# Kernel optimization log

Measured on AMD Instinct MI355X. Metric: run time of the kernel, lower is better.

Reference implementation:

```python
import jax, jax.numpy as jnp
import numpy as np

ROPE_THETA = 500000.0


def apply_rope(x, position_ids):
    # x: (B, H, S, hd), position_ids: (B, S)
    hd = x.shape[-1]
    inv_freq = 1.0 / (ROPE_THETA ** (jnp.arange(0, hd, 2, dtype=x.dtype) / hd))  # (hd/2,)
    freqs = position_ids.astype(x.dtype)[:, :, None] * inv_freq  # (B, S, hd/2)
    sin = jnp.sin(freqs)[:, None, :, :]  # (B, 1, S, hd/2)
    cos = jnp.cos(freqs)[:, None, :, :]
    x1 = x[..., ::2]
    x2 = x[..., 1::2]
    even = x1 * cos - x2 * sin
    odd = x2 * cos + x1 * sin
    # interleave even/odd back: stack on a new trailing axis then flatten
    return jnp.stack([even, odd], axis=-1).reshape(x.shape)


def setup_inputs() -> dict:
    key = jax.random.key(0)
    k_x, k_q, k_k, k_v, k_o = jax.random.split(key, 5)
    B, S, D = 2, 2048, 2048
    H, H_kv = 32, 8
    hd = D // H
    x = jax.random.normal(k_x, (B, S, D), dtype=jnp.float32)
    position_ids = jnp.broadcast_to(jnp.arange(S, dtype=jnp.int64)[None, :], (B, S))
    scale = 0.02
    Wq = jax.random.normal(k_q, (D, H * hd), dtype=jnp.float32) * scale
    Wk = jax.random.normal(k_k, (D, H_kv * hd), dtype=jnp.float32) * scale
    Wv = jax.random.normal(k_v, (D, H_kv * hd), dtype=jnp.float32) * scale
    Wo = jax.random.normal(k_o, (D, D), dtype=jnp.float32) * scale
    return {"x": x, "position_ids": position_ids, "Wq": Wq, "Wk": Wk, "Wv": Wv, "Wo": Wo}


def reference(x, position_ids, Wq, Wk, Wv, Wo):
    B, S, D = x.shape
    H, H_kv = 32, 8
    hd = D // H
    G = H // H_kv  # query heads per kv head

    q = (x @ Wq).reshape(B, S, H, hd).transpose(0, 2, 1, 3)        # (B, H, S, hd)
    k = (x @ Wk).reshape(B, S, H_kv, hd).transpose(0, 2, 1, 3)     # (B, H_kv, S, hd)
    v = (x @ Wv).reshape(B, S, H_kv, hd).transpose(0, 2, 1, 3)

    q = apply_rope(q, position_ids)
    k = apply_rope(k, position_ids)

    # GQA: group query heads (B, H_kv, G, S, hd); repeat_interleave maps head h -> kv head h // G
    qg = q.reshape(B, H_kv, G, S, hd)
    scores = jnp.einsum("bkgsh,bkth->bkgst", qg, k) / jnp.sqrt(jnp.asarray(hd, x.dtype))

    causal = jnp.triu(jnp.ones((S, S), dtype=bool), 1)  # True = masked
    scores = jnp.where(causal, jnp.asarray(-jnp.inf, scores.dtype), scores)

    attn = jax.nn.softmax(scores, axis=-1)  # (B, H_kv, G, S, S)
    z = jnp.einsum("bkgst,bkth->bkgsh", attn, v)  # (B, H_kv, G, S, hd)
    z = z.reshape(B, H, S, hd).transpose(0, 2, 1, 3).reshape(B, S, D)
    return z @ Wo
```

## Files before the change

### kernel.cpp

```cpp
#include <hip/hip_runtime.h>
#include <hip/hip_bf16.h>


#define S_LEN 2048
#define DIM   2048
#define NH    32
#define NKV   8
#define HD    64
#define BS    4096
#define NQKV  3072
#define LL(x) ((long long)(x))

typedef __bf16 bf16x8 __attribute__((ext_vector_type(8)));
typedef float  f32x4  __attribute__((ext_vector_type(4)));
typedef float  f32x16 __attribute__((ext_vector_type(16)));
typedef unsigned u32x4 __attribute__((ext_vector_type(4)));

__device__ __forceinline__ unsigned short bfb(float f) {
  __hip_bfloat16 h = __float2bfloat16(f);
  return *reinterpret_cast<unsigned short*>(&h);
}

__device__ __forceinline__ unsigned cvtpk(float lo, float hi) {
  unsigned u;
  asm("v_cvt_pk_bf16_f32 %0, %1, %2" : "=v"(u) : "v"(lo), "v"(hi));
  return u;
}

__device__ __forceinline__ void gload16(const void* g, void* l) {
  __builtin_amdgcn_global_load_lds(
      (const __attribute__((address_space(1))) void*)g,
      (__attribute__((address_space(3))) void*)l, 16, 0, 0);
}

__device__ __forceinline__ void tcast_body(
    const float* __restrict__ in, unsigned short* __restrict__ out,
    int K, int N, int bx, int by, int tid, float* tile ) {
  int n0 = bx * 32, k0 = by * 32;
  int tx = tid & 31, ty = tid >> 5;
#pragma unroll
  for (int r = 0; r < 32; r += 8)
    tile[(ty + r) * 33 + tx] = in[LL(k0 + ty + r) * N + n0 + tx];
  __syncthreads();
#pragma unroll
  for (int r = 0; r < 32; r += 8)
    out[LL(n0 + ty + r) * K + k0 + tx] = bfb(tile[tx * 33 + ty + r]);
}

__global__ __launch_bounds__(256) void k_prep(
    const float* __restrict__ x,  const float* __restrict__ Wq,
    const float* __restrict__ Wk, const float* __restrict__ Wv,
    const float* __restrict__ Wo, float* __restrict__ tab,
    unsigned short* __restrict__ xb, unsigned short* __restrict__ wqkvt,
    unsigned short* __restrict__ wot) {
  __shared__ float tile[32 * 33];
  int blk = blockIdx.x, tid = threadIdx.x;
  if (blk < 256) {
    int i = blk * 256 + tid;
    int s = i >> 5, f = i & 31;
    double inv = pow(500000.0, -2.0 * (double)f / 64.0);
    double fr = (double)s * inv;
    tab[2 * i]     = (float)cos(fr);
    tab[2 * i + 1] = (float)sin(fr);
  } else if (blk < 8448) {
    int i = (blk - 256) * 256 + tid;
    float4 v = ((const float4*)x)[i];
    ushort4 o;
    o.x = bfb(v.x); o.y = bfb(v.y); o.z = bfb(v.z); o.w = bfb(v.w);
    ((ushort4*)xb)[i] = o;
  } else if (blk < 12544) {
    int t2 = blk - 8448;
    tcast_body(Wq, wqkvt, DIM, DIM, t2 & 63, t2 >> 6, tid, tile);
  } else if (blk < 13568) {
    int t3 = blk - 12544;
    tcast_body(Wk, wqkvt + LL(2048) * DIM, DIM, 512, t3 & 15, t3 >> 4, tid, tile);
  } else if (blk < 14592) {
    int t4 = blk - 13568;
    tcast_body(Wv, wqkvt + LL(2560) * DIM, DIM, 512, t4 & 15, t4 >> 4, tid, tile);
  } else {
    int t5 = blk - 14592;
    tcast_body(Wo, wot, DIM, DIM, t5 & 63, t5 >> 6, tid, tile);
  }
}

template <int MODE>
__global__ __launch_bounds__(256, 2) void k_gemm(
    const unsigned short* __restrict__ A, const unsigned short* __restrict__ Bt,
    void* __restrict__ Cout, int M, int N, int K,
    const float* __restrict__ tab, unsigned short* __restrict__ qbuf,
    unsigned short* __restrict__ kbuf, unsigned short* __restrict__ vtb) {
  __shared__ __align__(16) unsigned short As[128 * 32];
  __shared__ __align__(16) unsigned short Bs[128 * 32];
  int t = threadIdx.x;
  int lane = t & 63, w = t >> 6;
  int wr = w >> 1, wc = w & 1;
  int g = lane >> 4, r = lane & 15;
  int gx = gridDim.x;
  int nwg = gx * gridDim.y;
  int lin = blockIdx.y * gx + blockIdx.x;
  int cpx = nwg >> 3;
  int swz = (lin & 7) * cpx + (lin >> 3);
  int bx = swz % gx, by = swz / gx;
  long long rowBase = LL(by) * 128;
  long long colBase = LL(bx) * 128;

  f32x4 acc[4][4] = {};

  int c0 = t, c1 = t + 256;
  const unsigned short* ag0 = A + (rowBase + (c0 >> 2)) * K + (c0 & 3) * 8;
  const unsigned short* ag1 = A + (rowBase + (c1 >> 2)) * K + (c1 & 3) * 8;
  const unsigned short* bg0 = Bt + (colBase + (c0 >> 2)) * K + (c0 & 3) * 8;
  const unsigned short* bg1 = Bt + (colBase + (c1 >> 2)) * K + (c1 & 3) * 8;
  char* lA0 = (char*)As + c0 * 16; char* lA1 = (char*)As + c1 * 16;
  char* lB0 = (char*)Bs + c0 * 16; char* lB1 = (char*)Bs + c1 * 16;

  for (int kt = 0; kt < K; kt += 32) {
    __syncthreads();
    gload16(ag0 + kt, lA0);
    gload16(ag1 + kt, lA1);
    gload16(bg0 + kt, lB0);
    gload16(bg1 + kt, lB1);
    __syncthreads();

    bf16x8 af[4], bfr[4];
#pragma unroll
    for (int m = 0; m < 4; m++)
      af[m] = *(const bf16x8*)(const void*)(As + (wr * 64 + m * 16 + r) * 32 + g * 8);
#pragma unroll
    for (int n = 0; n < 4; n++)
      bfr[n] = *(const bf16x8*)(const void*)(Bs + (wc * 64 + n * 16 + r) * 32 + g * 8);
#pragma unroll
    for (int m = 0; m < 4; m++)
#pragma unroll
      for (int n = 0; n < 4; n++)
        acc[m][n] = __builtin_amdgcn_mfma_f32_16x16x32_bf16(af[m], bfr[n], acc[m][n], 0, 0, 0);
  }

  if (MODE == 0) {
#pragma unroll
    for (int m = 0; m < 4; m++)
#pragma unroll
      for (int n = 0; n < 4; n++) {
        long long row0 = rowBase + wr * 64 + m * 16 + g * 4;
        long long col = colBase + wc * 64 + n * 16 + r;
#pragma unroll
        for (int j = 0; j < 4; j++)
          ((float*)Cout)[(row0 + j) * N + col] = acc[m][n][j];
      }
  } else {
#pragma unroll
    for (int n = 0; n < 4; n++) {
      int gc0 = (int)colBase + wc * 64 + n * 16;
      int gc = gc0 + r;
      if (gc0 < 2560) {
        unsigned short* dst; int dcol, dstride; float scale;
        if (gc0 < 2048) { dst = qbuf; dcol = gc;        dstride = DIM; scale = 0.18033688f; }
        else            { dst = kbuf; dcol = gc - 2048; dstride = 512; scale = 1.0f; }
        int f = (gc & 63) >> 1;
        float sgn = (gc & 1) ? 1.f : -1.f;
#pragma unroll
        for (int m = 0; m < 4; m++) {
          long long row0 = rowBase + wr * 64 + m * 16 + g * 4;
#pragma unroll
          for (int j = 0; j < 4; j++) {
            float v = acc[m][n][j];
            float part = __shfl_xor(v, 1);
            int s = (int)((row0 + j) & (S_LEN - 1));
            float cc = tab[(s * 32 + f) * 2], ss = tab[(s * 32 + f) * 2 + 1];
            float o = (v * cc + sgn * part * ss) * scale;
            dst[(row0 + j) * dstride + dcol] = bfb(o);
          }
        }
      } else {
        int dcol = gc - 2560;
#pragma unroll
        for (int m = 0; m < 4; m++) {
          long long row0 = rowBase + wr * 64 + m * 16 + g * 4;
#pragma unroll
          for (int j = 0; j < 4; j++) {
            long long row = row0 + j;
            long long bq = row >> 11;
            int s = (int)(row & (S_LEN - 1));
            vtb[(bq * 512 + dcol) * S_LEN + s] = bfb(acc[m][n][j]);
          }
        }
      }
    }
  }
}

__global__ __launch_bounds__(256, 2) void k_attn(
    const unsigned short* __restrict__ qb, const unsigned short* __restrict__ kb,
    const unsigned short* __restrict__ vt, unsigned short* __restrict__ zb) {
  int lin = blockIdx.x + 16 * (blockIdx.y + 32 * blockIdx.z);
  int kvh = lin & 7;
  int idx = lin >> 3;
  int st = 15 - (idx >> 3);
  int b = (idx >> 2) & 1;
  int h = kvh * 4 + (idx & 3);
  int bh = b * NKV + kvh;

  int t = threadIdx.x, lane = t & 63, w = t >> 6;
  int l31 = lane & 31, hi = lane >> 5;
  int sw = (l31 & 7) * 8;

  __shared__ __align__(16) unsigned short Ks[2][64 * 64];
  __shared__ __align__(16) unsigned short Vs[2][64 * 64];

  int c0 = t, c1 = t + 256;
  const unsigned short* kg0 = kb + LL(b) * S_LEN * 512 + (c0 >> 3) * 512 + kvh * HD
                                 + (((c0 & 7) ^ ((c0 >> 3) & 7)) * 8);
  const unsigned short* kg1 = kb + LL(b) * S_LEN * 512 + (c1 >> 3) * 512 + kvh * HD
                                 + (((c1 & 7) ^ ((c1 >> 3) & 7)) * 8);
  const unsigned short* vg0 = vt + (LL(bh) * HD + (c0 >> 3)) * S_LEN
                                 + (((c0 & 7) ^ ((c0 >> 3) & 7)) * 8);
  const unsigned short* vg1 = vt + (LL(bh) * HD + (c1 >> 3)) * S_LEN
                                 + (((c1 & 7) ^ ((c1 >> 3) & 7)) * 8);

#define STAGE(bufi, kst_)                                              \
  {                                                                    \
    gload16(kg0 + LL(kst_) * 512, (char*)Ks[bufi] + c0 * 16);          \
    gload16(kg1 + LL(kst_) * 512, (char*)Ks[bufi] + c1 * 16);          \
    gload16(vg0 + (kst_), (char*)Vs[bufi] + c0 * 16);                  \
    gload16(vg1 + (kst_), (char*)Vs[bufi] + c1 * 16);                  \
  }

  int rowb = st * 128 + w * 32;
  int qg = rowb + l31;
  long long qrow = LL(b) * S_LEN + qg;

  bf16x8 qf[4];
#pragma unroll
  for (int s = 0; s < 4; s++)
    qf[s] = *(const bf16x8*)(const void*)(qb + qrow * DIM + h * HD + s * 16 + hi * 8);

  f32x16 acc0 = {}, acc1 = {};
  float mrun = -1e30f, lrun = 0.f;

  int nt = 2 * st + 2;
  STAGE(0, 0);
  for (int tt = 0; tt < nt; tt++) {
    int kst = tt * 64;
    int cur = tt & 1;
    asm volatile("s_waitcnt vmcnt(0)" ::: "memory");
    __builtin_amdgcn_s_barrier();
    __builtin_amdgcn_sched_barrier(0);
    if (tt + 1 < nt) STAGE(cur ^ 1, kst + 64);

    if (kst <= rowb + 31) {
      const unsigned short* Kc = Ks[cur];
      const unsigned short* Vc = Vs[cur];

      bf16x8 kf[2][4];
#pragma unroll
      for (int kbi = 0; kbi < 2; kbi++)
#pragma unroll
        for (int s = 0; s < 4; s++)
          kf[kbi][s] = *(const bf16x8*)(const void*)(
              Kc + (kbi * 32 + l31) * 64 + ((s * 16 + hi * 8) ^ sw));

      __builtin_amdgcn_s_setprio(1);
      f32x16 sc0 = {}, sc1 = {};
#pragma unroll
      for (int s = 0; s < 4; s++) {
        sc0 = __builtin_amdgcn_mfma_f32_32x32x16_bf16(kf[0][s], qf[s], sc0, 0, 0, 0);
        sc1 = __builtin_amdgcn_mfma_f32_32x32x16_bf16(kf[1][s], qf[s], sc1, 0, 0, 0);
      }
      __builtin_amdgcn_s_setprio(0);

      bf16x8 vf[8];
#pragma unroll
      for (int db = 0; db < 2; db++)
#pragma unroll
        for (int f = 0; f < 4; f++)
          vf[db * 4 + f] = *(const bf16x8*)(const void*)(
              Vc + (db * 32 + l31) * 64 + ((f * 16 + hi * 8) ^ sw));

      if (kst + 63 > rowb) {
#pragma unroll
        for (int q = 0; q < 16; q++) {
          int kl = (q & 3) + 8 * (q >> 2) + 4 * hi;
          if (kst + kl > qg) sc0[q] = -1e30f;
          if (kst + 32 + kl > qg) sc1[q] = -1e30f;
        }
      }

      float pm = -1e30f;
#pragma unroll
      for (int q = 0; q < 16; q++) {
        pm = fmaxf(pm, sc0[q]);
        pm = fmaxf(pm, sc1[q]);
      }
      pm = fmaxf(pm, __shfl_xor(pm, 32));
      if (__any(pm > mrun + 12.0f)) {
        float mnew = fmaxf(mrun, pm);
        float al = exp2f(mrun - mnew);
        mrun = mnew;
        lrun *= al;
        acc0 *= al;
        acc1 *= al;
      }
      f32x16 pv0, pv1;
      float ls = 0.f;
#pragma unroll
      for (int q = 0; q < 16; q++) {
        pv0[q] = exp2f(sc0[q] - mrun);
        pv1[q] = exp2f(sc1[q] - mrun);
        ls += pv0[q] + pv1[q];
      }
      lrun += ls + __shfl_xor(ls, 32);

      bf16x8 pfr[4];
#pragma unroll
      for (int f = 0; f < 4; f++) {
        int qb_ = (f & 1) * 8;
        float e0, e1, e2, e3, e4, e5, e6, e7;
        if (f < 2) {
          e0 = pv0[qb_ + 0]; e1 = pv0[qb_ + 1]; e2 = pv0[qb_ + 2]; e3 = pv0[qb_ + 3];
          e4 = pv0[qb_ + 4]; e5 = pv0[qb_ + 5]; e6 = pv0[qb_ + 6]; e7 = pv0[qb_ + 7];
        } else {
          e0 = pv1[qb_ + 0]; e1 = pv1[qb_ + 1]; e2 = pv1[qb_ + 2]; e3 = pv1[qb_ + 3];
          e4 = pv1[qb_ + 4]; e5 = pv1[qb_ + 5]; e6 = pv1[qb_ + 6]; e7 = pv1[qb_ + 7];
        }
        unsigned a0 = cvtpk(e0, e1), a1 = cvtpk(e2, e3);
        unsigned b0 = cvtpk(e4, e5), b1 = cvtpk(e6, e7);
        asm volatile("v_permlane32_swap_b32 %0, %1" : "+v"(a0), "+v"(b0));
        asm volatile("v_permlane32_swap_b32 %0, %1" : "+v"(a1), "+v"(b1));
        u32x4 uu;
        uu[0] = a0;
        uu[1] = a1;
        uu[2] = b0;
        uu[3] = b1;
        pfr[f] = *(bf16x8*)&uu;
      }

      __builtin_amdgcn_s_setprio(1);
#pragma unroll
      for (int f = 0; f < 4; f++) {
        acc0 = __builtin_amdgcn_mfma_f32_32x32x16_bf16(vf[f],     pfr[f], acc0, 0, 0, 0);
        acc1 = __builtin_amdgcn_mfma_f32_32x32x16_bf16(vf[4 + f], pfr[f], acc1, 0, 0, 0);
      }
      __builtin_amdgcn_s_setprio(0);
    }
  }

  float invl = 1.0f / lrun;
#pragma unroll
  for (int q4 = 0; q4 < 4; q4++) {
    uint2 u;
    u.x = cvtpk(acc0[q4 * 4 + 0] * invl, acc0[q4 * 4 + 1] * invl);
    u.y = cvtpk(acc0[q4 * 4 + 2] * invl, acc0[q4 * 4 + 3] * invl);
    *(uint2*)(void*)(zb + qrow * DIM + h * HD + 8 * q4 + 4 * hi) = u;
    uint2 v;
    v.x = cvtpk(acc1[q4 * 4 + 0] * invl, acc1[q4 * 4 + 1] * invl);
    v.y = cvtpk(acc1[q4 * 4 + 2] * invl, acc1[q4 * 4 + 3] * invl);
    *(uint2*)(void*)(zb + qrow * DIM + h * HD + 32 + 8 * q4 + 4 * hi) = v;
  }
#undef STAGE
}

extern "C" void kernel_launch(void* const* d_in, const int* in_sizes, int n_in,
                              void* d_out, int out_size, void* d_ws, size_t ws_size,
                              hipStream_t stream) {
  const float* x  = (const float*)d_in[0];
  const float* Wq = (const float*)d_in[2];
  const float* Wk = (const float*)d_in[3];
  const float* Wv = (const float*)d_in[4];
  const float* Wo = (const float*)d_in[5];
  float* out = (float*)d_out;

  char* wsb = (char*)d_ws;
  size_t off = 0;
  auto alloc = [&](size_t bytes) {
    void* p = wsb + off;
    off += (bytes + 255) & ~(size_t)255;
    return p;
  };
  float* tab            = (float*)alloc(LL(S_LEN) * 32 * 2 * 4);
  unsigned short* xb    = (unsigned short*)alloc(LL(BS) * DIM * 2);
  unsigned short* wqkvt = (unsigned short*)alloc(LL(NQKV) * DIM * 2);
  unsigned short* wot   = (unsigned short*)alloc(LL(DIM) * DIM * 2);
  unsigned short* qbuf  = (unsigned short*)alloc(LL(BS) * DIM * 2);
  unsigned short* kbuf  = (unsigned short*)alloc(LL(BS) * (NKV * HD) * 2);
  unsigned short* vtb   = (unsigned short*)alloc(LL(2 * NKV) * HD * S_LEN * 2);
  unsigned short* zb    = (unsigned short*)alloc(LL(BS) * DIM * 2);

  k_prep<<<18688, 256, 0, stream>>>(x, Wq, Wk, Wv, Wo, tab, xb, wqkvt, wot);

  k_gemm<2><<<dim3(NQKV / 128, BS / 128), 256, 0, stream>>>(
      xb, wqkvt, nullptr, BS, NQKV, DIM, tab, qbuf, kbuf, vtb);

  k_attn<<<dim3(16, NH, 2), 256, 0, stream>>>(qbuf, kbuf, vtb, zb);

  k_gemm<0><<<dim3(DIM / 128, BS / 128), 256, 0, stream>>>(
      zb, wot, out, BS, DIM, DIM, nullptr, nullptr, nullptr, nullptr);
}
```

Measured before the change: 195.2 us.

## Double GEMM K-tile to 64 with XOR-swizzled LDS layout

Raises the GEMM K step from 32 to 64, so each tile loads four 16-byte chunks per thread per operand and runs two MFMA sub-steps between barriers. This halves the number of barrier pairs and loop iterations. The LDS rows are stored XOR-swizzled by source column to avoid bank conflicts on the wider 128-byte rows. LDS use doubles to 32KB per block, which may limit occupancy under the 2-blocks launch bound.

```diff
diff --git a/kernel.cpp b/kernel.cpp
--- a/kernel.cpp
+++ b/kernel.cpp
@@ -89,12 +89,13 @@
     void* __restrict__ Cout, int M, int N, int K,
     const float* __restrict__ tab, unsigned short* __restrict__ qbuf,
     unsigned short* __restrict__ kbuf, unsigned short* __restrict__ vtb) {
-  __shared__ __align__(16) unsigned short As[128 * 32];
-  __shared__ __align__(16) unsigned short Bs[128 * 32];
+  __shared__ __align__(16) unsigned short As[128 * 64];
+  __shared__ __align__(16) unsigned short Bs[128 * 64];
   int t = threadIdx.x;
   int lane = t & 63, w = t >> 6;
   int wr = w >> 1, wc = w & 1;
   int g = lane >> 4, r = lane & 15;
+  int sw = (r & 7) * 8;
   int gx = gridDim.x;
   int nwg = gx * gridDim.y;
   int lin = blockIdx.y * gx + blockIdx.x;
@@ -106,34 +107,52 @@
 
   f32x4 acc[4][4] = {};
 
-  int c0 = t, c1 = t + 256;
-  const unsigned short* ag0 = A + (rowBase + (c0 >> 2)) * K + (c0 & 3) * 8;
-  const unsigned short* ag1 = A + (rowBase + (c1 >> 2)) * K + (c1 & 3) * 8;
-  const unsigned short* bg0 = Bt + (colBase + (c0 >> 2)) * K + (c0 & 3) * 8;
-  const unsigned short* bg1 = Bt + (colBase + (c1 >> 2)) * K + (c1 & 3) * 8;
+  int c0 = t, c1 = t + 256, c2 = t + 512, c3 = t + 768;
+#define SRCP(P, base, c) ((P) + ((base) + ((c) >> 3)) * K \
+                               + ((((c) & 7) ^ (((c) >> 3) & 7)) * 8))
+  const unsigned short* ag0 = SRCP(A, rowBase, c0);
+  const unsigned short* ag1 = SRCP(A, rowBase, c1);
+  const unsigned short* ag2 = SRCP(A, rowBase, c2);
+  const unsigned short* ag3 = SRCP(A, rowBase, c3);
+  const unsigned short* bg0 = SRCP(Bt, colBase, c0);
+  const unsigned short* bg1 = SRCP(Bt, colBase, c1);
+  const unsigned short* bg2 = SRCP(Bt, colBase, c2);
+  const unsigned short* bg3 = SRCP(Bt, colBase, c3);
+#undef SRCP
   char* lA0 = (char*)As + c0 * 16; char* lA1 = (char*)As + c1 * 16;
+  char* lA2 = (char*)As + c2 * 16; char* lA3 = (char*)As + c3 * 16;
   char* lB0 = (char*)Bs + c0 * 16; char* lB1 = (char*)Bs + c1 * 16;
-
-  for (int kt = 0; kt < K; kt += 32) {
+  char* lB2 = (char*)Bs + c2 * 16; char* lB3 = (char*)Bs + c3 * 16;
+
+  for (int kt = 0; kt < K; kt += 64) {
     __syncthreads();
     gload16(ag0 + kt, lA0);
     gload16(ag1 + kt, lA1);
+    gload16(ag2 + kt, lA2);
+    gload16(ag3 + kt, lA3);
     gload16(bg0 + kt, lB0);
     gload16(bg1 + kt, lB1);
+    gload16(bg2 + kt, lB2);
+    gload16(bg3 + kt, lB3);
     __syncthreads();
 
-    bf16x8 af[4], bfr[4];
-#pragma unroll
-    for (int m = 0; m < 4; m++)
-      af[m] = *(const bf16x8*)(const void*)(As + (wr * 64 + m * 16 + r) * 32 + g * 8);
-#pragma unroll
-    for (int n = 0; n < 4; n++)
-      bfr[n] = *(const bf16x8*)(const void*)(Bs + (wc * 64 + n * 16 + r) * 32 + g * 8);
-#pragma unroll
-    for (int m = 0; m < 4; m++)
+#pragma unroll
+    for (int kd = 0; kd < 2; kd++) {
+      bf16x8 af[4], bfr[4];
+#pragma unroll
+      for (int m = 0; m < 4; m++)
+        af[m] = *(const bf16x8*)(const void*)(
+            As + (wr * 64 + m * 16 + r) * 64 + ((kd * 32 + g * 8) ^ sw));
 #pragma unroll
       for (int n = 0; n < 4; n++)
-        acc[m][n] = __builtin_amdgcn_mfma_f32_16x16x32_bf16(af[m], bfr[n], acc[m][n], 0, 0, 0);
+        bfr[n] = *(const bf16x8*)(const void*)(
+            Bs + (wc * 64 + n * 16 + r) * 64 + ((kd * 32 + g * 8) ^ sw));
+#pragma unroll
+      for (int m = 0; m < 4; m++)
+#pragma unroll
+        for (int n = 0; n < 4; n++)
+          acc[m][n] = __builtin_amdgcn_mfma_f32_16x16x32_bf16(af[m], bfr[n], acc[m][n], 0, 0, 0);
+    }
   }
 
   if (MODE == 0) {
```

After: 187.9 us (median of 2 runs). 1.04x faster.
